# Optimization experiments

Hardware: AMD Instinct MI355X
Metric: run time of the kernel (lower is better)

Reference implementation:

```python
import jax, jax.numpy as jnp
import numpy as np

N = 1024    # number of graph nodes
DIM = 64    # embedding dim (structure2vec paper uses 64)
T = 4       # message-passing rounds


def setup_inputs() -> dict:
    key = jax.random.key(0)
    ks = jax.random.split(key, 9)
    s = np.float32(1.0 / np.sqrt(DIM))
    x = jax.random.randint(ks[0], (N,), 0, 2).astype(jnp.float32)        # node indicator (v in S)
    graph = jax.random.normal(ks[1], (N, N), dtype=jnp.float32)          # dense edge weights w(v, v')
    W1 = jax.random.normal(ks[2], (DIM,), dtype=jnp.float32) * s         # theta1: Linear(1, dim)
    W2 = jax.random.normal(ks[3], (DIM, DIM), dtype=jnp.float32) * s     # theta2
    W3 = jax.random.normal(ks[4], (DIM, DIM), dtype=jnp.float32) * s     # theta3
    W4 = jax.random.normal(ks[5], (DIM,), dtype=jnp.float32) * s         # theta4: Linear(1, dim)
    W5 = jax.random.normal(ks[6], (2 * DIM,), dtype=jnp.float32) * s     # theta5: Linear(2*dim, 1)
    W6 = jax.random.normal(ks[7], (DIM, DIM), dtype=jnp.float32) * s     # theta6
    W7 = jax.random.normal(ks[8], (DIM, DIM), dtype=jnp.float32) * s     # theta7
    return {"x": x, "graph": graph, "W1": W1, "W2": W2, "W3": W3,
            "W4": W4, "W5": W5, "W6": W6, "W7": W7, "v": 7}


def reference(x, graph, W1, W2, W3, W4, W5, W6, W7, v):
    # ---- loop-invariant terms (graph and x are fixed across rounds) ----
    # per-edge embedding: relu(theta4 * w(i,k)) summed over k  -> [N, DIM]
    M = jnp.sum(jax.nn.relu(graph[:, :, None] * W4[None, None, :]), axis=1)
    t3 = M @ W3.T                      # theta3(sum_k relu(theta4 * w))      [N, DIM]
    t1 = x[:, None] * W1[None, :]      # theta1 * x_v                        [N, DIM]

    # ---- structure2vec rounds: u_v <- relu(t1 + theta2 * (sum_u' u_u' - u_v) + t3) ----
    u = jnp.zeros((x.shape[0], W1.shape[0]), dtype=x.dtype)   # [N, DIM]
    for _ in range(T):
        summ = jnp.sum(u, axis=0)                    # [DIM] sum over all nodes
        t2 = (summ[None, :] - u) @ W2.T              # exclude self           [N, DIM]
        u = jax.nn.relu(t1 + t2 + t3)

    # ---- Q(v) = theta5 . relu([theta6 * sum_u u_u ; theta7 * u_v]) ----
    h = jax.nn.relu(jnp.concatenate([W6 @ jnp.sum(u, axis=0), W7 @ u[v]]))
    return jnp.dot(W5, h)
```

## Files before the change

### kernel.cpp

```cpp
#include <hip/hip_runtime.h>

#define NN 1024
#define DIM 64
#define NB 128
#define NT 512

typedef unsigned int u32;

#define S1 0x51F0A001u
#define S2 0x51F0A002u
#define S3 0x51F0A003u
#define S4 0x51F0A004u

__device__ __forceinline__ void slot_store(u32* p, float v) {
    union { float f; u32 u; } c; c.f = v;
    __hip_atomic_store(p, c.u, __ATOMIC_RELAXED, __HIP_MEMORY_SCOPE_AGENT);
}
__device__ __forceinline__ float slot_load(const u32* p) {
    union { u32 u; float f; } c;
    c.u = __hip_atomic_load(p, __ATOMIC_RELAXED, __HIP_MEMORY_SCOPE_AGENT);
    return c.f;
}
__device__ __forceinline__ u32 flag_load(const u32* p) {
    return __hip_atomic_load(p, __ATOMIC_RELAXED, __HIP_MEMORY_SCOPE_AGENT);
}
__device__ __forceinline__ void flag_store(u32* p, u32 v) {
    __hip_atomic_store(p, v, __ATOMIC_RELAXED, __HIP_MEMORY_SCOPE_AGENT);
}

__device__ __forceinline__ void poll_all(const u32* flags, u32 sense, int lane) {
    for (;;) {
        const u32 v0 = flag_load(&flags[lane * 16]);
        const u32 v1 = flag_load(&flags[(64 + lane) * 16]);
        if (__all((v0 == sense) && (v1 == sense))) break;
        __builtin_amdgcn_s_sleep(1);
    }
}

__global__ __launch_bounds__(NT) void s2v(
    const float* __restrict__ x, const float* __restrict__ graph,
    const float* __restrict__ W1, const float* __restrict__ W2,
    const float* __restrict__ W3, const float* __restrict__ W4,
    const float* __restrict__ W5, const float* __restrict__ W6,
    const float* __restrict__ W7, const int* __restrict__ vptr,
    float* __restrict__ out,
    u32* __restrict__ flagA, u32* __restrict__ flagB,
    u32* __restrict__ slots,
    u32* __restrict__ uvg)
{
    __shared__ float w2t[DIM * 65];
    __shared__ float uloc[8 * DIM];
    __shared__ float part[8][DIM];
    __shared__ float part2[8][DIM];
    __shared__ float pcol[8][DIM];
    __shared__ float w4s[DIM], c1s[DIM], c2s[DIM];
    __shared__ float su[DIM], uv[DIM];

    const int t = threadIdx.x, lane = t & 63, wave = t >> 6;
    const int b = blockIdx.x;
    const int v = vptr[0];

    #pragma unroll
    for (int k = 0; k < 8; ++k) {
        const int idx = t + NT * k;
        w2t[(idx & 63) * 65 + (idx >> 6)] = W2[idx];
    }
    if (t < DIM) w4s[t] = W4[t];
    __syncthreads();

    float pos = 0.f, neg = 0.f;
    {
        const float* row = graph + (size_t)(b * 8 + wave) * NN;
        #pragma unroll
        for (int k = 0; k < 4; ++k) {
            float4 g = *reinterpret_cast<const float4*>(row + 4 * lane + 256 * k);
            pos += fmaxf(g.x,0.f)+fmaxf(g.y,0.f)+fmaxf(g.z,0.f)+fmaxf(g.w,0.f);
            neg += fminf(g.x,0.f)+fminf(g.y,0.f)+fminf(g.z,0.f)+fminf(g.w,0.f);
        }
        #pragma unroll
        for (int m = 32; m >= 1; m >>= 1) {
            pos += __shfl_xor(pos, m, 64);
            neg += __shfl_xor(neg, m, 64);
        }
    }
    if (t < DIM) {
        float a1 = 0.f, a2 = 0.f;
        const float* w3r = W3 + t * DIM;
        #pragma unroll 8
        for (int e = 0; e < DIM; ++e) {
            a1 += w3r[e] * fmaxf(w4s[e], 0.f);
            a2 += w3r[e] * fminf(w4s[e], 0.f);
        }
        c1s[t] = a1; c2s[t] = a2;
    }
    __syncthreads();

    float br, ur;
    {
        const float xv = x[b * 8 + wave];
        br = xv * W1[lane] + pos * c1s[lane] + neg * c2s[lane];
        ur = fmaxf(br, 0.f);
        uloc[wave * DIM + lane] = ur;
        pcol[wave][lane] = ur;
    }
    __syncthreads();

    if (wave == 0) {
        float ps = 0.f;
        #pragma unroll
        for (int w = 0; w < 8; ++w) ps += pcol[w][lane];
        slot_store(&slots[(size_t)(0 * NB + b) * DIM + lane], ps);
        asm volatile("s_waitcnt vmcnt(0)" ::: "memory");
        if (lane == 0) flag_store(&flagA[b * 16], S1);
        poll_all(flagA, S1, lane);
    }
    __syncthreads();

    #pragma unroll 1
    for (int r = 0; r < 3; ++r) {
        {
            float s = 0.f;
            #pragma unroll
            for (int j = 0; j < 16; ++j)
                s += slot_load(&slots[(size_t)(r * NB + wave * 16 + j) * DIM + lane]);
            part[wave][lane] = s;
        }
        __syncthreads();
        {
            float qp = 0.f;
            #pragma unroll
            for (int k = 0; k < 8; ++k) {
                const int e = wave * 8 + k;
                const float se = part[0][e] + part[1][e] + part[2][e] + part[3][e]
                               + part[4][e] + part[5][e] + part[6][e] + part[7][e];
                qp += w2t[e * 65 + lane] * se;
            }
            part2[wave][lane] = qp;
        }
        __syncthreads();
        const float q = part2[0][lane] + part2[1][lane] + part2[2][lane] + part2[3][lane]
                      + part2[4][lane] + part2[5][lane] + part2[6][lane] + part2[7][lane];
        float acc = 0.f;
        #pragma unroll 8
        for (int e = 0; e < DIM; ++e)
            acc += w2t[e * 65 + lane] * uloc[wave * DIM + e];
        ur = fmaxf(br + q - acc, 0.f);
        uloc[wave * DIM + lane] = ur;
        pcol[wave][lane] = ur;

        if (r == 2 && b == (v >> 3) && wave == (v & 7)) {
            slot_store(&uvg[lane], ur);
            asm volatile("s_waitcnt vmcnt(0)" ::: "memory");
        }
        __syncthreads();

        if (wave == 0) {
            float ps = 0.f;
            #pragma unroll
            for (int w = 0; w < 8; ++w) ps += pcol[w][lane];
            slot_store(&slots[(size_t)((r + 1) * NB + b) * DIM + lane], ps);
            asm volatile("s_waitcnt vmcnt(0)" ::: "memory");
        }
        if (r == 0) {
            if (wave == 0) {
                if (lane == 0) flag_store(&flagB[b * 16], S2);
                poll_all(flagB, S2, lane);
            }
            __syncthreads();
        } else if (r == 1) {
            if (wave == 0) {
                if (lane == 0) flag_store(&flagA[b * 16], S3);
                poll_all(flagA, S3, lane);
            }
            __syncthreads();
        }
    }

    if (wave == 0 && lane == 0) flag_store(&flagB[b * 16], S4);
    if (b != 0) return;
    if (wave == 0) poll_all(flagB, S4, lane);
    __syncthreads();

    {
        float s = 0.f;
        #pragma unroll
        for (int j = 0; j < 16; ++j)
            s += slot_load(&slots[(size_t)(3 * NB + wave * 16 + j) * DIM + lane]);
        part[wave][lane] = s;
    }
    __syncthreads();
    if (t < DIM) {
        su[t] = part[0][t] + part[1][t] + part[2][t] + part[3][t]
              + part[4][t] + part[5][t] + part[6][t] + part[7][t];
        uv[t] = slot_load(&uvg[t]);
    }
    __syncthreads();
    if (t < DIM) {
        float h1 = 0.f, h2 = 0.f;
        const float* w6r = W6 + t * DIM;
        const float* w7r = W7 + t * DIM;
        #pragma unroll 8
        for (int e = 0; e < DIM; ++e) {
            h1 += w6r[e] * su[e];
            h2 += w7r[e] * uv[e];
        }
        float val = W5[t] * fmaxf(h1, 0.f) + W5[DIM + t] * fmaxf(h2, 0.f);
        #pragma unroll
        for (int m = 32; m >= 1; m >>= 1) val += __shfl_xor(val, m, 64);
        if (t == 0) out[0] = val;
    }
}

extern "C" void kernel_launch(void* const* d_in, const int* in_sizes, int n_in,
                              void* d_out, int out_size, void* d_ws, size_t ws_size,
                              hipStream_t stream) {
    const float* x     = (const float*)d_in[0];
    const float* graph = (const float*)d_in[1];
    const float* W1    = (const float*)d_in[2];
    const float* W2    = (const float*)d_in[3];
    const float* W3    = (const float*)d_in[4];
    const float* W4    = (const float*)d_in[5];
    const float* W5    = (const float*)d_in[6];
    const float* W6    = (const float*)d_in[7];
    const float* W7    = (const float*)d_in[8];
    const int*   vptr  = (const int*)d_in[9];
    float* out = (float*)d_out;

    unsigned char* ws = (unsigned char*)d_ws;
    u32* flagA = (u32*)ws;
    u32* flagB = (u32*)(ws + 8192);
    u32* slots = (u32*)(ws + 16384);
    u32* uvg   = (u32*)(ws + 16384 + 131072);

    s2v<<<NB, NT, 0, stream>>>(x, graph, W1, W2, W3, W4, W5, W6, W7,
                               vptr, out, flagA, flagB, slots, uvg);
}
```

Before: 23.93 us.

## Pack barrier flags contiguously and issue graph row loads before weight staging

Barrier flags drop their 64-byte stride and sit in adjacent words, so each polling wave reads all 128 flags from a few cache lines rather than 128 separate lines. The graph-row float4 loads are also issued at kernel entry, before the W2 transpose and W3 preprocessing, so their latency overlaps that setup. The trade-off is that many blocks now write flags into the same cache lines, which may cause contention on stores, and the early loads raise register pressure.

After: 30.47 us. 1.27x slower.

```diff
diff --git a/kernel.cpp b/kernel.cpp
--- a/kernel.cpp
+++ b/kernel.cpp
@@ -30,8 +30,8 @@
 
 __device__ __forceinline__ void poll_all(const u32* flags, u32 sense, int lane) {
     for (;;) {
-        const u32 v0 = flag_load(&flags[lane * 16]);
-        const u32 v1 = flag_load(&flags[(64 + lane) * 16]);
+        const u32 v0 = flag_load(&flags[lane]);
+        const u32 v1 = flag_load(&flags[64 + lane]);
         if (__all((v0 == sense) && (v1 == sense))) break;
         __builtin_amdgcn_s_sleep(1);
     }
@@ -60,6 +60,12 @@
     const int b = blockIdx.x;
     const int v = vptr[0];
 
+    const float* row = graph + (size_t)(b * 8 + wave) * NN;
+    float4 g0 = *reinterpret_cast<const float4*>(row + 4 * lane);
+    float4 g1 = *reinterpret_cast<const float4*>(row + 4 * lane + 256);
+    float4 g2 = *reinterpret_cast<const float4*>(row + 4 * lane + 512);
+    float4 g3 = *reinterpret_cast<const float4*>(row + 4 * lane + 768);
+
     #pragma unroll
     for (int k = 0; k < 8; ++k) {
         const int idx = t + NT * k;
@@ -68,21 +74,6 @@
     if (t < DIM) w4s[t] = W4[t];
     __syncthreads();
 
-    float pos = 0.f, neg = 0.f;
-    {
-        const float* row = graph + (size_t)(b * 8 + wave) * NN;
-        #pragma unroll
-        for (int k = 0; k < 4; ++k) {
-            float4 g = *reinterpret_cast<const float4*>(row + 4 * lane + 256 * k);
-            pos += fmaxf(g.x,0.f)+fmaxf(g.y,0.f)+fmaxf(g.z,0.f)+fmaxf(g.w,0.f);
-            neg += fminf(g.x,0.f)+fminf(g.y,0.f)+fminf(g.z,0.f)+fminf(g.w,0.f);
-        }
-        #pragma unroll
-        for (int m = 32; m >= 1; m >>= 1) {
-            pos += __shfl_xor(pos, m, 64);
-            neg += __shfl_xor(neg, m, 64);
-        }
-    }
     if (t < DIM) {
         float a1 = 0.f, a2 = 0.f;
         const float* w3r = W3 + t * DIM;
@@ -93,6 +84,24 @@
         }
         c1s[t] = a1; c2s[t] = a2;
     }
+
+    float pos, neg;
+    {
+        float p0 = fmaxf(g0.x,0.f)+fmaxf(g0.y,0.f)+fmaxf(g0.z,0.f)+fmaxf(g0.w,0.f)
+                 + fmaxf(g1.x,0.f)+fmaxf(g1.y,0.f)+fmaxf(g1.z,0.f)+fmaxf(g1.w,0.f)
+                 + fmaxf(g2.x,0.f)+fmaxf(g2.y,0.f)+fmaxf(g2.z,0.f)+fmaxf(g2.w,0.f)
+                 + fmaxf(g3.x,0.f)+fmaxf(g3.y,0.f)+fmaxf(g3.z,0.f)+fmaxf(g3.w,0.f);
+        float n0 = fminf(g0.x,0.f)+fminf(g0.y,0.f)+fminf(g0.z,0.f)+fminf(g0.w,0.f)
+                 + fminf(g1.x,0.f)+fminf(g1.y,0.f)+fminf(g1.z,0.f)+fminf(g1.w,0.f)
+                 + fminf(g2.x,0.f)+fminf(g2.y,0.f)+fminf(g2.z,0.f)+fminf(g2.w,0.f)
+                 + fminf(g3.x,0.f)+fminf(g3.y,0.f)+fminf(g3.z,0.f)+fminf(g3.w,0.f);
+        #pragma unroll
+        for (int m = 32; m >= 1; m >>= 1) {
+            p0 += __shfl_xor(p0, m, 64);
+            n0 += __shfl_xor(n0, m, 64);
+        }
+        pos = p0; neg = n0;
+    }
     __syncthreads();
 
     float br, ur;
@@ -111,7 +120,7 @@
         for (int w = 0; w < 8; ++w) ps += pcol[w][lane];
         slot_store(&slots[(size_t)(0 * NB + b) * DIM + lane], ps);
         asm volatile("s_waitcnt vmcnt(0)" ::: "memory");
-        if (lane == 0) flag_store(&flagA[b * 16], S1);
+        if (lane == 0) flag_store(&flagA[b], S1);
         poll_all(flagA, S1, lane);
     }
     __syncthreads();
@@ -163,20 +172,20 @@
         }
         if (r == 0) {
             if (wave == 0) {
-                if (lane == 0) flag_store(&flagB[b * 16], S2);
+                if (lane == 0) flag_store(&flagB[b], S2);
                 poll_all(flagB, S2, lane);
             }
             __syncthreads();
         } else if (r == 1) {
             if (wave == 0) {
-                if (lane == 0) flag_store(&flagA[b * 16], S3);
+                if (lane == 0) flag_store(&flagA[b], S3);
                 poll_all(flagA, S3, lane);
             }
             __syncthreads();
         }
     }
 
-    if (wave == 0 && lane == 0) flag_store(&flagB[b * 16], S4);
+    if (wave == 0 && lane == 0) flag_store(&flagB[b], S4);
     if (b != 0) return;
     if (wave == 0) poll_all(flagB, S4, lane);
     __syncthreads();
@@ -228,9 +237,9 @@
 
     unsigned char* ws = (unsigned char*)d_ws;
     u32* flagA = (u32*)ws;
-    u32* flagB = (u32*)(ws + 8192);
-    u32* slots = (u32*)(ws + 16384);
-    u32* uvg   = (u32*)(ws + 16384 + 131072);
+    u32* flagB = (u32*)(ws + 1024);
+    u32* slots = (u32*)(ws + 4096);
+    u32* uvg   = (u32*)(ws + 4096 + 131072);
 
     s2v<<<NB, NT, 0, stream>>>(x, graph, W1, W2, W3, W4, W5, W6, W7,
                                vptr, out, flagA, flagB, slots, uvg);
```
